# Kernel tuning notes

Measured on AMD Instinct MI355X. Metric: run time of the kernel, lower is better.

## Reference

```python
import jax, jax.numpy as jnp
import numpy as np

NUM_CLASSES = 1000
FEAT_DIM = 128
BATCH = 1_000_000


def setup_inputs() -> dict:
    key = jax.random.key(0)
    k1, k2, k3 = jax.random.split(key, 3)
    x = jax.random.normal(k1, (BATCH, FEAT_DIM), dtype=jnp.float32)
    labels = jax.random.randint(k2, (BATCH,), 0, NUM_CLASSES, dtype=jnp.int32)
    centers = jax.random.normal(k3, (NUM_CLASSES, FEAT_DIM), dtype=jnp.float32)
    return {"x": x, "labels": labels, "centers": centers}


def reference(x, labels, centers):
    # margin = ||centers[0] - centers[1]|| / 10, computed from detached centers at init
    margin = jax.lax.stop_gradient(jnp.sqrt(jnp.sum((centers[0] - centers[1]) ** 2)) / 10.0)
    # gather the center for each sample: (N, d)
    cb = centers[labels]
    # per-sample squared euclidean distance == diag of the original's N x N addmm matrix
    d = jnp.sum(x * x, axis=1) + jnp.sum(cb * cb, axis=1) - 2.0 * jnp.sum(x * cb, axis=1)
    hinge = jnp.maximum(jnp.float32(0.0), d - margin)
    batch_size = x.shape[0]
    return jnp.sum(hinge) / (batch_size * 2 * 2)
```

## Files before the change

### kernel.cpp

```cpp
#include <hip/hip_runtime.h>
#include <math.h>

#define N_BATCH 1000000
#define FEAT 128
#define FEAT4 32
#define GRID_MAIN 2048
#define BLOCK_MAIN 256
#define GROUPS_PER_BLOCK 8
#define ROW_STRIDE (GRID_MAIN * GROUPS_PER_BLOCK)


__global__ void nh_precompute(const float* __restrict__ centers,
                              float* __restrict__ margin_out) {
    int lane = threadIdx.x;
    float s = 0.0f;
    for (int k = lane; k < FEAT; k += 64) {
        float d = centers[k] - centers[FEAT + k];
        s += d * d;
    }
    #pragma unroll
    for (int m = 32; m >= 1; m >>= 1) s += __shfl_xor(s, m);
    if (lane == 0) {
        *margin_out = sqrtf(s) * 0.1f;
    }
}

__global__ __launch_bounds__(BLOCK_MAIN)
void nh_main(const float4* __restrict__ x,
             const int* __restrict__ labels,
             const float4* __restrict__ centers,
             const float* __restrict__ margin_p,
             float* __restrict__ partials) {
    const float margin = *margin_p;
    const int lane32 = threadIdx.x & 31;
    const int group  = threadIdx.x >> 5;

    float local = 0.0f;
    int row = blockIdx.x * GROUPS_PER_BLOCK + group;

    for (; row + ROW_STRIDE < N_BATCH; row += 2 * ROW_STRIDE) {
        const int r1 = row + ROW_STRIDE;
        const int l0 = labels[row];
        const int l1 = labels[r1];
        const float4 xv0 = x[(size_t)row * FEAT4 + lane32];
        const float4 xv1 = x[(size_t)r1  * FEAT4 + lane32];
        const float4 cv0 = centers[(size_t)l0 * FEAT4 + lane32];
        const float4 cv1 = centers[(size_t)l1 * FEAT4 + lane32];

        float d0 = xv0.x - cv0.x; float s0 = d0 * d0;
        float d1 = xv1.x - cv1.x; float s1 = d1 * d1;
        d0 = xv0.y - cv0.y; s0 = fmaf(d0, d0, s0);
        d1 = xv1.y - cv1.y; s1 = fmaf(d1, d1, s1);
        d0 = xv0.z - cv0.z; s0 = fmaf(d0, d0, s0);
        d1 = xv1.z - cv1.z; s1 = fmaf(d1, d1, s1);
        d0 = xv0.w - cv0.w; s0 = fmaf(d0, d0, s0);
        d1 = xv1.w - cv1.w; s1 = fmaf(d1, d1, s1);

        #pragma unroll
        for (int m = 16; m >= 1; m >>= 1) {
            s0 += __shfl_xor(s0, m);
            s1 += __shfl_xor(s1, m);
        }
        if (lane32 == 0) {
            float h0 = s0 - margin; local += (h0 > 0.0f) ? h0 : 0.0f;
            float h1 = s1 - margin; local += (h1 > 0.0f) ? h1 : 0.0f;
        }
    }
    if (row < N_BATCH) {
        const int l0 = labels[row];
        const float4 xv0 = x[(size_t)row * FEAT4 + lane32];
        const float4 cv0 = centers[(size_t)l0 * FEAT4 + lane32];
        float d0 = xv0.x - cv0.x; float s0 = d0 * d0;
        d0 = xv0.y - cv0.y; s0 = fmaf(d0, d0, s0);
        d0 = xv0.z - cv0.z; s0 = fmaf(d0, d0, s0);
        d0 = xv0.w - cv0.w; s0 = fmaf(d0, d0, s0);
        #pragma unroll
        for (int m = 16; m >= 1; m >>= 1) s0 += __shfl_xor(s0, m);
        if (lane32 == 0) {
            float h0 = s0 - margin; local += (h0 > 0.0f) ? h0 : 0.0f;
        }
    }

    #pragma unroll
    for (int m = 32; m >= 1; m >>= 1) local += __shfl_xor(local, m);
    __shared__ float wavesum[BLOCK_MAIN / 64];
    const int wid = threadIdx.x >> 6;
    if ((threadIdx.x & 63) == 0) wavesum[wid] = local;
    __syncthreads();
    if (threadIdx.x == 0) {
        float t = 0.0f;
        #pragma unroll
        for (int w = 0; w < BLOCK_MAIN / 64; ++w) t += wavesum[w];
        partials[blockIdx.x] = t;
    }
}

__global__ __launch_bounds__(256)
void nh_finalize(const float* __restrict__ partials, float* __restrict__ out) {
    float s = 0.0f;
    for (int i = threadIdx.x; i < GRID_MAIN; i += 256) s += partials[i];
    #pragma unroll
    for (int m = 32; m >= 1; m >>= 1) s += __shfl_xor(s, m);
    __shared__ float wavesum[4];
    const int wid = threadIdx.x >> 6;
    if ((threadIdx.x & 63) == 0) wavesum[wid] = s;
    __syncthreads();
    if (threadIdx.x == 0) {
        float t = wavesum[0] + wavesum[1] + wavesum[2] + wavesum[3];
        out[0] = t * (1.0f / ((float)N_BATCH * 4.0f));
    }
}

extern "C" void kernel_launch(void* const* d_in, const int* in_sizes, int n_in,
                              void* d_out, int out_size, void* d_ws, size_t ws_size,
                              hipStream_t stream) {
    const float* x       = (const float*)d_in[0];
    const int*   labels  = (const int*)d_in[1];
    const float* centers = (const float*)d_in[2];
    float* out = (float*)d_out;

    float* margin   = (float*)d_ws;
    float* partials = (float*)((char*)d_ws + 16);

    nh_precompute<<<1, 64, 0, stream>>>(centers, margin);
    nh_main<<<GRID_MAIN, BLOCK_MAIN, 0, stream>>>(
        (const float4*)x, labels, (const float4*)centers, margin, partials);
    nh_finalize<<<1, 256, 0, stream>>>(partials, out);
}
```

Baseline: 657.1 us.

## Process contiguous 8-row chunks per group and fuse margin and finalize into main kernel

Each 32-lane group now handles 8 consecutive rows per iteration, issuing all label, x and center loads up front for more memory-level parallelism and contiguous access. The margin is recomputed inside every group instead of in a separate precompute kernel, and the final reduction uses a float atomicAdd into the output after a tiny init kernel, which removes the finalize launch. In exchange the summation order is nondeterministic, and N_BATCH must be divisible by 8, which holds here.

```diff
diff --git a/kernel.cpp b/kernel.cpp
--- a/kernel.cpp
+++ b/kernel.cpp
@@ -2,112 +2,90 @@
 #include <math.h>
 
 #define N_BATCH 1000000
-#define FEAT 128
 #define FEAT4 32
 #define GRID_MAIN 2048
 #define BLOCK_MAIN 256
 #define GROUPS_PER_BLOCK 8
-#define ROW_STRIDE (GRID_MAIN * GROUPS_PER_BLOCK)
+#define N_GROUPS (GRID_MAIN * GROUPS_PER_BLOCK)
+#define RPC 8
+#define N_CHUNKS (N_BATCH / RPC)
 
-
-__global__ void nh_precompute(const float* __restrict__ centers,
-                              float* __restrict__ margin_out) {
-    int lane = threadIdx.x;
-    float s = 0.0f;
-    for (int k = lane; k < FEAT; k += 64) {
-        float d = centers[k] - centers[FEAT + k];
-        s += d * d;
-    }
-    #pragma unroll
-    for (int m = 32; m >= 1; m >>= 1) s += __shfl_xor(s, m);
-    if (lane == 0) {
-        *margin_out = sqrtf(s) * 0.1f;
-    }
-}
+__global__ void nh_init(float* __restrict__ out) { out[0] = 0.0f; }
 
 __global__ __launch_bounds__(BLOCK_MAIN)
 void nh_main(const float4* __restrict__ x,
              const int* __restrict__ labels,
              const float4* __restrict__ centers,
-             const float* __restrict__ margin_p,
-             float* __restrict__ partials) {
-    const float margin = *margin_p;
+             float* __restrict__ out) {
     const int lane32 = threadIdx.x & 31;
-    const int group  = threadIdx.x >> 5;
+    const int gid = blockIdx.x * GROUPS_PER_BLOCK + (threadIdx.x >> 5);
+
+    {
+    }
+    float4 a = centers[lane32];
+    float4 b = centers[FEAT4 + lane32];
+    float d = a.x - b.x; float ms = d * d;
+    d = a.y - b.y; ms = fmaf(d, d, ms);
+    d = a.z - b.z; ms = fmaf(d, d, ms);
+    d = a.w - b.w; ms = fmaf(d, d, ms);
+    #pragma unroll
+    for (int m = 16; m >= 1; m >>= 1) ms += __shfl_xor(ms, m);
+    const float margin = sqrtf(ms) * 0.1f;
 
     float local = 0.0f;
-    int row = blockIdx.x * GROUPS_PER_BLOCK + group;
 
-    for (; row + ROW_STRIDE < N_BATCH; row += 2 * ROW_STRIDE) {
-        const int r1 = row + ROW_STRIDE;
-        const int l0 = labels[row];
-        const int l1 = labels[r1];
-        const float4 xv0 = x[(size_t)row * FEAT4 + lane32];
-        const float4 xv1 = x[(size_t)r1  * FEAT4 + lane32];
-        const float4 cv0 = centers[(size_t)l0 * FEAT4 + lane32];
-        const float4 cv1 = centers[(size_t)l1 * FEAT4 + lane32];
+    for (int c = gid; c < N_CHUNKS; c += N_GROUPS) {
+        const int r0 = c * RPC;
 
-        float d0 = xv0.x - cv0.x; float s0 = d0 * d0;
-        float d1 = xv1.x - cv1.x; float s1 = d1 * d1;
-        d0 = xv0.y - cv0.y; s0 = fmaf(d0, d0, s0);
-        d1 = xv1.y - cv1.y; s1 = fmaf(d1, d1, s1);
-        d0 = xv0.z - cv0.z; s0 = fmaf(d0, d0, s0);
-        d1 = xv1.z - cv1.z; s1 = fmaf(d1, d1, s1);
-        d0 = xv0.w - cv0.w; s0 = fmaf(d0, d0, s0);
-        d1 = xv1.w - cv1.w; s1 = fmaf(d1, d1, s1);
+        const int* lp = labels + r0;
+        int lab[RPC];
+        #pragma unroll
+        for (int j = 0; j < RPC; ++j) lab[j] = lp[j];
+
+        const float4* xp = x + (size_t)r0 * FEAT4 + lane32;
+        float4 xv[RPC];
+        #pragma unroll
+        for (int j = 0; j < RPC; ++j) xv[j] = xp[j * FEAT4];
+
+        float4 cv[RPC];
+        #pragma unroll
+        for (int j = 0; j < RPC; ++j) cv[j] = centers[lab[j] * FEAT4 + lane32];
+
+        float s[RPC];
+        #pragma unroll
+        for (int j = 0; j < RPC; ++j) {
+            float t0 = xv[j].x - cv[j].x; float t = t0 * t0;
+            t0 = xv[j].y - cv[j].y; t = fmaf(t0, t0, t);
+            t0 = xv[j].z - cv[j].z; t = fmaf(t0, t0, t);
+            t0 = xv[j].w - cv[j].w; t = fmaf(t0, t0, t);
+            s[j] = t;
+        }
 
         #pragma unroll
         for (int m = 16; m >= 1; m >>= 1) {
-            s0 += __shfl_xor(s0, m);
-            s1 += __shfl_xor(s1, m);
+            #pragma unroll
+            for (int j = 0; j < RPC; ++j) s[j] += __shfl_xor(s[j], m);
         }
+
         if (lane32 == 0) {
-            float h0 = s0 - margin; local += (h0 > 0.0f) ? h0 : 0.0f;
-            float h1 = s1 - margin; local += (h1 > 0.0f) ? h1 : 0.0f;
-        }
-    }
-    if (row < N_BATCH) {
-        const int l0 = labels[row];
-        const float4 xv0 = x[(size_t)row * FEAT4 + lane32];
-        const float4 cv0 = centers[(size_t)l0 * FEAT4 + lane32];
-        float d0 = xv0.x - cv0.x; float s0 = d0 * d0;
-        d0 = xv0.y - cv0.y; s0 = fmaf(d0, d0, s0);
-        d0 = xv0.z - cv0.z; s0 = fmaf(d0, d0, s0);
-        d0 = xv0.w - cv0.w; s0 = fmaf(d0, d0, s0);
-        #pragma unroll
-        for (int m = 16; m >= 1; m >>= 1) s0 += __shfl_xor(s0, m);
-        if (lane32 == 0) {
-            float h0 = s0 - margin; local += (h0 > 0.0f) ? h0 : 0.0f;
+            #pragma unroll
+            for (int j = 0; j < RPC; ++j) {
+                float h = s[j] - margin;
+                local += (h > 0.0f) ? h : 0.0f;
+            }
         }
     }
 
     #pragma unroll
     for (int m = 32; m >= 1; m >>= 1) local += __shfl_xor(local, m);
     __shared__ float wavesum[BLOCK_MAIN / 64];
-    const int wid = threadIdx.x >> 6;
-    if ((threadIdx.x & 63) == 0) wavesum[wid] = local;
+    if ((threadIdx.x & 63) == 0) wavesum[threadIdx.x >> 6] = local;
     __syncthreads();
     if (threadIdx.x == 0) {
         float t = 0.0f;
         #pragma unroll
         for (int w = 0; w < BLOCK_MAIN / 64; ++w) t += wavesum[w];
-        partials[blockIdx.x] = t;
-    }
-}
-
-__global__ __launch_bounds__(256)
-void nh_finalize(const float* __restrict__ partials, float* __restrict__ out) {
-    float s = 0.0f;
-    for (int i = threadIdx.x; i < GRID_MAIN; i += 256) s += partials[i];
-    #pragma unroll
-    for (int m = 32; m >= 1; m >>= 1) s += __shfl_xor(s, m);
-    __shared__ float wavesum[4];
-    const int wid = threadIdx.x >> 6;
-    if ((threadIdx.x & 63) == 0) wavesum[wid] = s;
-    __syncthreads();
-    if (threadIdx.x == 0) {
-        float t = wavesum[0] + wavesum[1] + wavesum[2] + wavesum[3];
-        out[0] = t * (1.0f / ((float)N_BATCH * 4.0f));
+        atomicAdd(out, t * (1.0f / ((float)N_BATCH * 4.0f)));
     }
 }
 
@@ -119,11 +97,7 @@
     const float* centers = (const float*)d_in[2];
     float* out = (float*)d_out;
 
-    float* margin   = (float*)d_ws;
-    float* partials = (float*)((char*)d_ws + 16);
-
-    nh_precompute<<<1, 64, 0, stream>>>(centers, margin);
+    nh_init<<<1, 1, 0, stream>>>(out);
     nh_main<<<GRID_MAIN, BLOCK_MAIN, 0, stream>>>(
-        (const float4*)x, labels, (const float4*)centers, margin, partials);
-    nh_finalize<<<1, 256, 0, stream>>>(partials, out);
+        (const float4*)x, labels, (const float4*)centers, out);
 }
```

Result: no change. 647.0 us (-1.5%).
